# Optimization experiments

Hardware: AMD Instinct MI355X
Metric: run time of the kernel (lower is better)

The kernel has to match this reference:

```python
import jax, jax.numpy as jnp
import numpy as np

B_SZ, SEQ, D_MODEL = 2, 4096, 2048
EXPAND, D_STATE, D_CONV = 2, 16, 4
D_INNER = EXPAND * D_MODEL          # 4096
DT_RANK = -(-D_MODEL // 16)         # 128


def setup_inputs() -> dict:
    key = jax.random.key(0)
    ks = jax.random.split(key, 9)
    s = 0.02
    hidden_states = jax.random.normal(ks[0], (B_SZ, SEQ, D_MODEL), jnp.float32)
    W_in = jax.random.normal(ks[1], (2 * D_INNER, D_MODEL), jnp.float32) * s
    conv_w = jax.random.normal(ks[2], (D_INNER, D_CONV), jnp.float32) * 0.2
    conv_b = jnp.zeros((D_INNER,), jnp.float32)
    W_x = jax.random.normal(ks[3], (DT_RANK + 2 * D_STATE, D_INNER), jnp.float32) * s
    W_dt = jax.random.normal(ks[4], (D_INNER, DT_RANK), jnp.float32) * (DT_RANK ** -0.5)
    # dt bias so softplus(dt) ~ [1e-3, 0.1] as in Mamba init
    u = jax.random.uniform(ks[5], (D_INNER,), jnp.float32)
    dt = jnp.exp(u * (np.log(0.1) - np.log(1e-3)) + np.log(1e-3))
    dt_bias = dt + jnp.log(-jnp.expm1(-dt))  # inverse softplus
    # S4D-real init: A = -[1..d_state] per channel (kept negative for stability)
    A = -jnp.tile(jnp.arange(1.0, D_STATE + 1.0, dtype=jnp.float32), (D_INNER, 1))
    D = jnp.ones((D_INNER,), jnp.float32)
    W_out = jax.random.normal(ks[6], (D_MODEL, D_INNER), jnp.float32) * s
    return {"hidden_states": hidden_states, "W_in": W_in, "conv_w": conv_w,
            "conv_b": conv_b, "W_x": W_x, "W_dt": W_dt, "dt_bias": dt_bias,
            "A": A, "D": D, "W_out": W_out}


def _mamba_fwd(hidden_states, W_in, conv_w, conv_b, W_x, W_dt, dt_bias, A, D, W_out):
    # in_proj -> (B, L, 2*d_inner); split into x and gate z
    xz = jnp.einsum('bld,ed->ble', hidden_states, W_in)
    x, z = jnp.split(xz, 2, axis=-1)                    # (B,L,d_inner) each
    # causal depthwise conv1d over L (kernel d_conv), then SiLU
    d_conv = conv_w.shape[1]
    xp = jnp.pad(x, ((0, 0), (d_conv - 1, 0), (0, 0)))
    L = x.shape[1]
    xc = conv_b
    acc = jnp.zeros_like(x)
    for k in range(d_conv):                             # small fixed loop (4 taps)
        acc = acc + xp[:, k:k + L, :] * conv_w[:, k]
    x = jax.nn.silu(acc + conv_b)
    # x_proj -> dt_rank + 2*d_state
    ssm = jnp.einsum('bld,ed->ble', x, W_x)
    dt_r, Bm, Cm = jnp.split(ssm, [DT_RANK, DT_RANK + D_STATE], axis=-1)
    delta = jax.nn.softplus(jnp.einsum('blr,dr->bld', dt_r, W_dt) + dt_bias)
    # selective scan: h_t = exp(delta_t*A) h_{t-1} + delta_t*B_t*u_t ; y_t = C_t.h_t
    def step(state, inp):
        d_t, u_t, B_t, C_t = inp                        # (B,Di),(B,Di),(B,N),(B,N)
        dA = jnp.exp(d_t[..., None] * A)                # (B,Di,N)
        state = state * dA + (d_t * u_t)[..., None] * B_t[:, None, :]
        y = jnp.einsum('bdn,bn->bd', state, C_t)
        return state, y
    init = jnp.zeros((x.shape[0], D_INNER, D_STATE), jnp.float32)
    xs = (jnp.swapaxes(delta, 0, 1), jnp.swapaxes(x, 0, 1),
          jnp.swapaxes(Bm, 0, 1), jnp.swapaxes(Cm, 0, 1))
    _, ys = jax.lax.scan(step, init, xs)
    y = jnp.swapaxes(ys, 0, 1) + x * D                  # D skip connection
    y = y * jax.nn.silu(z)                              # gate
    return jnp.einsum('bld,md->blm', y, W_out)


def reference(hidden_states, W_in, conv_w, conv_b, W_x, W_dt, dt_bias, A, D, W_out):
    return _mamba_fwd(hidden_states, W_in, conv_w, conv_b, W_x, W_dt,
                      dt_bias, A, D, W_out)
```

## Files before the change

### kernel.cpp

```cpp
#include <hip/hip_runtime.h>
#include <hip/hip_bf16.h>
#include <cstdint>
#include <cstddef>

typedef _Float16 f16x8 __attribute__((ext_vector_type(8)));
typedef _Float16 f16x4 __attribute__((ext_vector_type(4)));
typedef float    f32x4 __attribute__((ext_vector_type(4)));

#define AS1 __attribute__((address_space(1)))
#define AS3 __attribute__((address_space(3)))

static constexpr int B_SZ = 2, SEQ = 4096, D_MODEL = 2048;
static constexpr int D_INNER = 4096, D_STATE = 16, D_CONV = 4, DT_RANK = 128;
static constexpr int M_ROWS = B_SZ * SEQ;
static constexpr int SSM_W  = DT_RANK + 2 * D_STATE;

__global__ __launch_bounds__(256) void k_cvt_f16(const float* __restrict__ in,
                                                 _Float16* __restrict__ out, int n4) {
    int i = blockIdx.x * 256 + threadIdx.x;
    if (i >= n4) return;
    f32x4 v = ((const f32x4*)in)[i];
    f16x4 h;
    h[0] = (_Float16)v[0]; h[1] = (_Float16)v[1];
    h[2] = (_Float16)v[2]; h[3] = (_Float16)v[3];
    ((f16x4*)out)[i] = h;
}

__global__ __launch_bounds__(256) void k_extract_dtr(const float* __restrict__ ssm,
                                                     _Float16* __restrict__ dtr) {
    int idx = blockIdx.x * 256 + threadIdx.x;
    if (idx >= M_ROWS * (DT_RANK / 4)) return;
    int m  = idx >> 5;
    int j4 = (idx & 31) * 4;
    f32x4 v = *(const f32x4*)&ssm[(size_t)m * SSM_W + j4];
    f16x4 h;
    h[0] = (_Float16)v[0]; h[1] = (_Float16)v[1];
    h[2] = (_Float16)v[2]; h[3] = (_Float16)v[3];
    *(f16x4*)&dtr[(size_t)m * DT_RANK + j4] = h;
}

template <int EPI>
__global__ __launch_bounds__(512, 2) void k_gemm256p(
    const _Float16* __restrict__ A, const _Float16* __restrict__ Bm, int K, int nby,
    void* __restrict__ out0, void* __restrict__ out1, int ldc) {
    __shared__ _Float16 lA[2][256][64];
    __shared__ _Float16 lB[2][256][64];
    constexpr int LBUF  = 32768;
    constexpr int LBUFH = 16384;

    const int tid = threadIdx.x, l = tid & 63, w = tid >> 6;
    const int fr = l & 15, fq = l >> 4;
    const int wrA = (w >> 2) * 128;
    const int wcB = (w & 3) * 64;

    const int nwg = gridDim.x, qq = nwg >> 3;
    const int id = (blockIdx.x & 7) * qq + (blockIdx.x >> 3);
    const int by = id % nby, bx = id / nby;
    const int tileM = by * 256, tileN = bx * 256;

    const int rsub = l >> 3;
    const int gco  = ((l & 7) ^ rsub) << 3;
    const int swz0 = (fq ^ (fr & 7)) << 4;

    const char* cA = (const char*)lA;
    const char* cB = (const char*)lB;
    const int bA0 = (wrA + fr) * 128 + swz0;
    const int bA1 = bA0 ^ 64;
    const int bB0 = (wcB + fr) * 128 + swz0;
    const int bB1 = bB0 ^ 64;

    const _Float16* pA[4];
    const _Float16* pB[4];
    _Float16* dA[4];
    _Float16* dB[4];
#pragma unroll
    for (int u = 0; u < 4; ++u) {
        const int brow = (u >> 1) * 128 + (w * 2 + (u & 1)) * 8;
        pA[u] = A  + (size_t)(tileM + brow + rsub) * K + gco;
        pB[u] = Bm + (size_t)(tileN + brow + rsub) * K + gco;
        dA[u] = &lA[0][brow][0];
        dB[u] = &lB[0][brow][0];
    }

    const int NK = K >> 6;

    f32x4 acc[8][4];
#pragma unroll
    for (int m = 0; m < 8; m++)
#pragma unroll
        for (int n = 0; n < 4; n++) acc[m][n] = (f32x4)0.f;

#pragma unroll
    for (int t = 0; t < 2; ++t) {
#pragma unroll
        for (int u = 0; u < 4; ++u)
            __builtin_amdgcn_global_load_lds((const AS1 void*)(pA[u] + t * 64),
                (AS3 void*)(dA[u] + t * LBUFH), 16, 0, 0);
#pragma unroll
        for (int u = 0; u < 4; ++u)
            __builtin_amdgcn_global_load_lds((const AS1 void*)(pB[u] + t * 64),
                (AS3 void*)(dB[u] + t * LBUFH), 16, 0, 0);
    }
#pragma unroll
    for (int u = 0; u < 4; ++u) { pA[u] += 128; pB[u] += 128; }
    asm volatile("s_waitcnt vmcnt(8)" ::: "memory");
    __builtin_amdgcn_s_barrier();

    f16x8 af[4][2], bf0[2][2], bf1[2][2];

#define MFMA_QUAD(MO, NO, BF)                                                        \
    __builtin_amdgcn_s_setprio(1);                                                   \
    _Pragma("unroll") for (int m = 0; m < 4; ++m)                                    \
    _Pragma("unroll") for (int n = 0; n < 2; ++n)                                    \
    _Pragma("unroll") for (int kk = 0; kk < 2; ++kk)                                 \
        acc[(MO) + m][(NO) + n] = __builtin_amdgcn_mfma_f32_16x16x32_f16(            \
            af[m][kk], BF[n][kk], acc[(MO) + m][(NO) + n], 0, 0, 0);                 \
    __builtin_amdgcn_s_setprio(0);

#define KTILE(BUF, KOFF, PF, DOEND)                                                  \
    _Pragma("unroll")                                                                \
    for (int m = 0; m < 4; ++m) {                                                    \
        af[m][0] = *(const f16x8*)(cA + (BUF) * LBUF + bA0 + m * 2048);              \
        af[m][1] = *(const f16x8*)(cA + (BUF) * LBUF + bA1 + m * 2048);              \
    }                                                                                \
    _Pragma("unroll")                                                                \
    for (int n = 0; n < 2; ++n) {                                                    \
        bf0[n][0] = *(const f16x8*)(cB + (BUF) * LBUF + bB0 + n * 2048);             \
        bf0[n][1] = *(const f16x8*)(cB + (BUF) * LBUF + bB1 + n * 2048);             \
    }                                                                                \
    __builtin_amdgcn_s_barrier();                                                    \
    asm volatile("s_waitcnt lgkmcnt(0)" ::: "memory");                               \
    __builtin_amdgcn_sched_barrier(0);                                               \
    MFMA_QUAD(0, 0, bf0)                                                             \
    __builtin_amdgcn_s_barrier();                                                    \
    _Pragma("unroll")                                                                \
    for (int n = 0; n < 2; ++n) {                                                    \
        bf1[n][0] = *(const f16x8*)(cB + (BUF) * LBUF + bB0 + (n + 2) * 2048);       \
        bf1[n][1] = *(const f16x8*)(cB + (BUF) * LBUF + bB1 + (n + 2) * 2048);       \
    }                                                                                \
    __builtin_amdgcn_s_barrier();                                                    \
    asm volatile("s_waitcnt lgkmcnt(0)" ::: "memory");                               \
    __builtin_amdgcn_sched_barrier(0);                                               \
    MFMA_QUAD(0, 2, bf1)                                                             \
    __builtin_amdgcn_s_barrier();                                                    \
    _Pragma("unroll")                                                                \
    for (int m = 0; m < 4; ++m) {                                                    \
        af[m][0] = *(const f16x8*)(cA + (BUF) * LBUF + bA0 + (m + 4) * 2048);        \
        af[m][1] = *(const f16x8*)(cA + (BUF) * LBUF + bA1 + (m + 4) * 2048);        \
    }                                                                                \
    if (PF) {                                                                        \
        _Pragma("unroll")                                                            \
        for (int u = 0; u < 4; ++u)                                                  \
            __builtin_amdgcn_global_load_lds((const AS1 void*)(pB[u] + (KOFF)),      \
                (AS3 void*)(dB[u] + (BUF) * LBUFH), 16, 0, 0);                       \
    }                                                                                \
    __builtin_amdgcn_s_barrier();                                                    \
    asm volatile("s_waitcnt lgkmcnt(0)" ::: "memory");                               \
    __builtin_amdgcn_sched_barrier(0);                                               \
    MFMA_QUAD(4, 0, bf0)                                                             \
    __builtin_amdgcn_s_barrier();                                                    \
    if (PF) {                                                                        \
        _Pragma("unroll")                                                            \
        for (int u = 0; u < 4; ++u)                                                  \
            __builtin_amdgcn_global_load_lds((const AS1 void*)(pA[u] + (KOFF)),      \
                (AS3 void*)(dA[u] + (BUF) * LBUFH), 16, 0, 0);                       \
    }                                                                                \
    __builtin_amdgcn_s_barrier();                                                    \
    MFMA_QUAD(4, 2, bf1)                                                             \
    if (DOEND) {                                                                     \
        if (PF) { asm volatile("s_waitcnt vmcnt(8)" ::: "memory"); }                 \
        else    { asm volatile("s_waitcnt vmcnt(0)" ::: "memory"); }                 \
        __builtin_amdgcn_s_barrier();                                                \
    }

    for (int kt = 0; kt < NK; kt += 2) {
        const bool pf0 = (kt + 2 < NK);
        const bool pf1 = (kt + 3 < NK);
        KTILE(0, 0, pf0, true)
        KTILE(1, 64, pf1, pf0)
#pragma unroll
        for (int u = 0; u < 4; ++u) { pA[u] += 128; pB[u] += 128; }
    }
#undef KTILE
#undef MFMA_QUAD

#pragma unroll
    for (int m = 0; m < 8; ++m) {
#pragma unroll
        for (int n = 0; n < 4; ++n) {
            const int r0 = tileM + wrA + m * 16 + fq * 4;
            const int c  = tileN + wcB + n * 16 + fr;
#pragma unroll
            for (int q = 0; q < 4; ++q) {
                const float  v  = acc[m][n][q];
                const size_t mm = (size_t)(r0 + q);
                if (EPI == 0) {
                    if (c < D_INNER)
                        ((_Float16*)out0)[mm * D_INNER + c] = (_Float16)v;
                    else
                        ((_Float16*)out1)[mm * D_INNER + (c - D_INNER)] = (_Float16)v;
                } else {
                    ((float*)out0)[mm * ldc + c] = v;
                }
            }
        }
    }
}

template <int BM, int BN, int EPI>
__global__ __launch_bounds__(256) void k_gemm_nt(
    const _Float16* __restrict__ A, const _Float16* __restrict__ Bm, int K,
    int lda, int ldb, void* __restrict__ out0,
    const float* __restrict__ bias, int ldc) {
    __shared__ _Float16 a_lds[BM][32];
    __shared__ _Float16 b_lds[BN][32];
    constexpr int MR = BM / 32;
    constexpr int NR = BN / 32;
    const int tid  = threadIdx.x;
    const int lane = tid & 63;
    const int wid  = tid >> 6;
    const int wr = wid >> 1, wc = wid & 1;
    const int tileM = blockIdx.y * BM;
    const int tileN = blockIdx.x * BN;

    f32x4 acc[MR][NR];
    for (int i = 0; i < MR; i++)
        for (int j = 0; j < NR; j++) acc[i][j] = (f32x4)0.f;

    constexpr int IS_A = BM / 16;
    constexpr int IS_B = BN / 16;
    const int srow = lane >> 2;
    const int skof = (lane & 3) * 8;
    const int fr = lane & 15, fq = lane >> 4;

    for (int kk = 0; kk < K; kk += 32) {
        if (kk) __syncthreads();
        for (int is = wid; is < IS_A + IS_B; is += 4) {
            const bool isA = is < IS_A;
            const int  li  = isA ? is : is - IS_A;
            const int  row = li * 16 + srow;
            const _Float16* g =
                isA ? (A  + (size_t)(tileM + row) * lda + kk + skof)
                    : (Bm + (size_t)(tileN + row) * ldb + kk + skof);
            char* lp = ((char*)(isA ? &a_lds[0][0] : &b_lds[0][0])) + (size_t)li * 1024;
            __builtin_amdgcn_global_load_lds((const AS1 void*)g, (AS3 void*)lp, 16, 0, 0);
        }
        __syncthreads();

        f16x8 af[MR], bf[NR];
#pragma unroll
        for (int i = 0; i < MR; i++)
            af[i] = *(const f16x8*)&a_lds[wr * (BM / 2) + i * 16 + fr][fq * 8];
#pragma unroll
        for (int j = 0; j < NR; j++)
            bf[j] = *(const f16x8*)&b_lds[wc * (BN / 2) + j * 16 + fr][fq * 8];
#pragma unroll
        for (int i = 0; i < MR; i++)
#pragma unroll
            for (int j = 0; j < NR; j++)
                acc[i][j] = __builtin_amdgcn_mfma_f32_16x16x32_f16(af[i], bf[j], acc[i][j], 0, 0, 0);
    }

#pragma unroll
    for (int i = 0; i < MR; i++) {
#pragma unroll
        for (int j = 0; j < NR; j++) {
            const int r0 = tileM + wr * (BM / 2) + i * 16 + fq * 4;
            const int c  = tileN + wc * (BN / 2) + j * 16 + fr;
#pragma unroll
            for (int q = 0; q < 4; q++) {
                const float  v = acc[i][j][q];
                const size_t m = (size_t)(r0 + q);
                if (EPI == 1) {
                    ((float*)out0)[m * ldc + c] = v;
                } else {
                    float x  = v + bias[c];
                    float sp = (x > 20.f) ? x : log1pf(__expf(x));
                    ((_Float16*)out0)[m * ldc + c] = (_Float16)sp;
                }
            }
        }
    }
}

__global__ __launch_bounds__(256) void k_conv_silu(const _Float16* __restrict__ x,
                                                   const float* __restrict__ w,
                                                   const float* __restrict__ bias,
                                                   _Float16* __restrict__ out) {
    const int idx = blockIdx.x * 256 + threadIdx.x;
    const int d4 = idx & (D_INNER / 4 - 1);
    const int t  = (idx >> 10) & (SEQ - 1);
    const int b  = idx >> 22;
    const int d  = d4 * 4;
    const size_t rowbase = (size_t)b * SEQ * D_INNER;

    f32x4 wv[4];
#pragma unroll
    for (int i = 0; i < 4; i++) wv[i] = ((const f32x4*)w)[d + i];

    float acc[4];
#pragma unroll
    for (int i = 0; i < 4; i++) acc[i] = bias[d + i];
#pragma unroll
    for (int k = 0; k < D_CONV; k++) {
        int ti = t - (D_CONV - 1) + k;
        if (ti < 0) continue;
        f16x4 xv = *(const f16x4*)&x[rowbase + (size_t)ti * D_INNER + d];
#pragma unroll
        for (int i = 0; i < 4; i++) acc[i] += (float)xv[i] * wv[i][k];
    }
    f16x4 o;
#pragma unroll
    for (int i = 0; i < 4; i++) {
        float v = acc[i];
        o[i] = (_Float16)(v / (1.f + __expf(-v)));
    }
    *(f16x4*)&out[rowbase + (size_t)t * D_INNER + d] = o;
}

template <int CH, typename ST>
__global__ __launch_bounds__(256) void k_scan_p1(const _Float16* __restrict__ delta_h,
                                                 const _Float16* __restrict__ xc,
                                                 const float* __restrict__ ssm,
                                                 const float* __restrict__ Aptr,
                                                 ST* __restrict__ Sbuf,
                                                 ST* __restrict__ Pbuf) {
    constexpr int NCH = SEQ / CH;
    constexpr float L2E = 1.44269504088896f;
    const int bid   = blockIdx.x;
    const int dg    = bid & 15;
    const int chunk = (bid >> 4) % NCH;
    const int b     = bid / (16 * NCH);
    const int d     = dg * 256 + threadIdx.x;

    __shared__ float bsh[CH][D_STATE];
    const size_t rb = (size_t)b * SEQ + (size_t)chunk * CH;
    for (int i = threadIdx.x; i < CH * D_STATE; i += 256) {
        int t = i >> 4, n = i & 15;
        bsh[t][n] = ssm[(rb + t) * SSM_W + DT_RANK + n];
    }
    __syncthreads();

    float a2[D_STATE];
#pragma unroll
    for (int n = 0; n < D_STATE; n++) a2[n] = Aptr[(size_t)d * D_STATE + n] * L2E;
    float st[D_STATE];
#pragma unroll
    for (int n = 0; n < D_STATE; n++) st[n] = 0.f;
    float dtsum = 0.f;

    for (int t = 0; t < CH; ++t) {
        const size_t idx = (rb + t) * D_INNER + d;
        const float dt = (float)delta_h[idx];
        const float u  = (float)xc[idx];
        const float du = dt * u;
        dtsum += dt;
#pragma unroll
        for (int n = 0; n < D_STATE; n++) {
            float p = exp2f(dt * a2[n]);
            st[n] = st[n] * p + du * bsh[t][n];
        }
    }
    const size_t ob = ((size_t)(b * NCH + chunk) * D_STATE) * D_INNER + d;
#pragma unroll
    for (int n = 0; n < D_STATE; n++) {
        Sbuf[ob + (size_t)n * D_INNER] = (ST)st[n];
        Pbuf[ob + (size_t)n * D_INNER] = (ST)exp2f(dtsum * a2[n]);
    }
}

template <int NCH, typename ST>
__global__ __launch_bounds__(256) void k_scan_p2(ST* __restrict__ Sbuf,
                                                 const ST* __restrict__ Pbuf) {
    const int id = blockIdx.x * 256 + threadIdx.x;
    const int d = id & (D_INNER - 1);
    const int n = (id >> 12) & 15;
    const int b = id >> 16;
    float h = 0.f;
    for (int c = 0; c < NCH; ++c) {
        const size_t off = ((size_t)((b * NCH + c) * D_STATE + n)) * D_INNER + d;
        const float Pv = (float)Pbuf[off];
        const float Sv = (float)Sbuf[off];
        Sbuf[off] = (ST)h;
        h = Pv * h + Sv;
    }
}

template <int CH, typename ST>
__global__ __launch_bounds__(256) void k_scan_p3(const _Float16* __restrict__ delta_h,
                                                 const _Float16* __restrict__ xc,
                                                 const float* __restrict__ ssm,
                                                 const _Float16* __restrict__ z,
                                                 const float* __restrict__ Aptr,
                                                 const float* __restrict__ Dptr,
                                                 const ST* __restrict__ Sbuf,
                                                 _Float16* __restrict__ y_out) {
    constexpr int NCH = SEQ / CH;
    constexpr float L2E = 1.44269504088896f;
    const int bid   = blockIdx.x;
    const int dg    = bid & 15;
    const int chunk = (bid >> 4) % NCH;
    const int b     = bid / (16 * NCH);
    const int d     = dg * 256 + threadIdx.x;

    __shared__ float bsh[CH][2 * D_STATE];
    const size_t rb = (size_t)b * SEQ + (size_t)chunk * CH;
    for (int i = threadIdx.x; i < CH * 2 * D_STATE; i += 256) {
        int t = i >> 5, j = i & 31;
        bsh[t][j] = ssm[(rb + t) * SSM_W + DT_RANK + j];
    }
    __syncthreads();

    float a2[D_STATE];
#pragma unroll
    for (int n = 0; n < D_STATE; n++) a2[n] = Aptr[(size_t)d * D_STATE + n] * L2E;
    const float Dd = Dptr[d];

    const size_t ob = ((size_t)(b * NCH + chunk) * D_STATE) * D_INNER + d;
    float st[D_STATE];
#pragma unroll
    for (int n = 0; n < D_STATE; n++) st[n] = (float)Sbuf[ob + (size_t)n * D_INNER];

    for (int t = 0; t < CH; ++t) {
        const size_t idx = (rb + t) * D_INNER + d;
        const float dt = (float)delta_h[idx];
        const float u  = (float)xc[idx];
        const float du = dt * u;
        float y = 0.f;
#pragma unroll
        for (int n = 0; n < D_STATE; n++) {
            float p = exp2f(dt * a2[n]);
            st[n] = st[n] * p + du * bsh[t][n];
            y += st[n] * bsh[t][D_STATE + n];
        }
        const float zv = (float)z[idx];
        const float g  = zv / (1.f + __expf(-zv));
        y_out[idx] = (_Float16)((y + u * Dd) * g);
    }
}

__global__ __launch_bounds__(256) void k_scan(const _Float16* __restrict__ delta_h,
                                              const _Float16* __restrict__ xc,
                                              const float* __restrict__ ssm,
                                              const _Float16* __restrict__ z,
                                              const float* __restrict__ Aptr,
                                              const float* __restrict__ Dptr,
                                              _Float16* __restrict__ y_out) {
    const int b = blockIdx.x >> 4;
    const int d = (blockIdx.x & 15) * 256 + threadIdx.x;
    constexpr float L2E = 1.44269504088896f;
    float a2[D_STATE];
#pragma unroll
    for (int n = 0; n < D_STATE; n++) a2[n] = Aptr[(size_t)d * D_STATE + n] * L2E;
    const float Dd = Dptr[d];
    float st[D_STATE];
#pragma unroll
    for (int n = 0; n < D_STATE; n++) st[n] = 0.f;
    __shared__ float bc[128][32];
    const size_t rb = (size_t)b * SEQ;
    for (int tc = 0; tc < SEQ; tc += 128) {
        __syncthreads();
        for (int i = threadIdx.x; i < 128 * 32; i += 256) {
            int tl = i >> 5, j = i & 31;
            bc[tl][j] = ssm[(rb + tc + tl) * SSM_W + DT_RANK + j];
        }
        __syncthreads();
        for (int tl = 0; tl < 128; ++tl) {
            const size_t idx = (rb + tc + tl) * D_INNER + d;
            const float dt = (float)delta_h[idx];
            const float u  = (float)xc[idx];
            const float du = dt * u;
            float y = 0.f;
#pragma unroll
            for (int n = 0; n < D_STATE; n++) {
                float dA = exp2f(dt * a2[n]);
                st[n] = st[n] * dA + du * bc[tl][n];
                y += st[n] * bc[tl][D_STATE + n];
            }
            const float zv = (float)z[idx];
            const float g  = zv / (1.f + __expf(-zv));
            y_out[idx] = (_Float16)((y + u * Dd) * g);
        }
    }
}

template <int CH, typename ST>
static void launch_chunked_scan(const _Float16* delta_h, const _Float16* xc,
                                const float* ssm, const _Float16* z,
                                const float* Aptr, const float* Dptr,
                                ST* S, ST* P, _Float16* y, hipStream_t stream) {
    constexpr int NCH = SEQ / CH;
    k_scan_p1<CH, ST><<<B_SZ * NCH * 16, 256, 0, stream>>>(delta_h, xc, ssm, Aptr, S, P);
    k_scan_p2<NCH, ST><<<(B_SZ * 16 * D_INNER) / 256, 256, 0, stream>>>(S, P);
    k_scan_p3<CH, ST><<<B_SZ * NCH * 16, 256, 0, stream>>>(delta_h, xc, ssm, z, Aptr, Dptr, S, y);
}

extern "C" void kernel_launch(void* const* d_in, const int* in_sizes, int n_in,
                              void* d_out, int out_size, void* d_ws, size_t ws_size,
                              hipStream_t stream) {
    const float* hs    = (const float*)d_in[0];
    const float* W_in  = (const float*)d_in[1];
    const float* convw = (const float*)d_in[2];
    const float* convb = (const float*)d_in[3];
    const float* W_x   = (const float*)d_in[4];
    const float* W_dt  = (const float*)d_in[5];
    const float* dtb   = (const float*)d_in[6];
    const float* Aptr  = (const float*)d_in[7];
    const float* Dptr  = (const float*)d_in[8];
    const float* W_out = (const float*)d_in[9];

    char* ws = (char*)d_ws;
    _Float16* hs_h    = (_Float16*)(ws + 0);
    _Float16* Win_h   = (_Float16*)(ws + 33554432);
    _Float16* y_h     = (_Float16*)(ws + 0);
    _Float16* xraw    = (_Float16*)(ws + 67108864);
    _Float16* delta_h = (_Float16*)(ws + 67108864);
    _Float16* xc      = (_Float16*)(ws + 134217728);
    float*    ssm     = (float*)   (ws + 201326592);
    _Float16* dtr     = (_Float16*)(ws + 206569472);
    _Float16* Wx_h    = (_Float16*)(ws + 208666624);
    _Float16* Wdt_h   = (_Float16*)(ws + 209977344);
    _Float16* Wout_h  = (_Float16*)(ws + 211025920);
    _Float16* z_h     = (_Float16*)d_out;
    const size_t spbase = 227803136ull;

    auto cvt = [&](const float* in, _Float16* out, int n) {
        int n4 = n / 4;
        k_cvt_f16<<<(n4 + 255) / 256, 256, 0, stream>>>(in, out, n4);
    };
    cvt(hs,    hs_h,   B_SZ * SEQ * D_MODEL);
    cvt(W_in,  Win_h,  2 * D_INNER * D_MODEL);
    cvt(W_x,   Wx_h,   SSM_W * D_INNER);
    cvt(W_dt,  Wdt_h,  D_INNER * DT_RANK);
    cvt(W_out, Wout_h, D_MODEL * D_INNER);

    k_gemm256p<0><<<(M_ROWS / 256) * (2 * D_INNER / 256), 512, 0, stream>>>(
        hs_h, Win_h, D_MODEL, M_ROWS / 256, xraw, z_h, 0);

    k_conv_silu<<<(B_SZ * SEQ * (D_INNER / 4)) / 256, 256, 0, stream>>>(xraw, convw, convb, xc);

    k_gemm_nt<128, 32, 1><<<dim3(SSM_W / 32, M_ROWS / 128), 256, 0, stream>>>(
        xc, Wx_h, D_INNER, D_INNER, D_INNER, ssm, nullptr, SSM_W);

    k_extract_dtr<<<(M_ROWS * (DT_RANK / 4)) / 256, 256, 0, stream>>>(ssm, dtr);

    k_gemm_nt<128, 128, 2><<<dim3(D_INNER / 128, M_ROWS / 128), 256, 0, stream>>>(
        dtr, Wdt_h, DT_RANK, DT_RANK, DT_RANK, delta_h, dtb, D_INNER);

    {
        const size_t e64  = (size_t)B_SZ * (SEQ / 64)  * D_STATE * D_INNER;
        const size_t e128 = (size_t)B_SZ * (SEQ / 128) * D_STATE * D_INNER;
        if (ws_size >= spbase + 2 * e64 * sizeof(float)) {
            float* S = (float*)(ws + spbase);
            float* P = S + e64;
            launch_chunked_scan<64, float>(delta_h, xc, ssm, z_h, Aptr, Dptr, S, P, y_h, stream);
        } else if (ws_size >= spbase + 2 * e128 * sizeof(float)) {
            float* S = (float*)(ws + spbase);
            float* P = S + e128;
            launch_chunked_scan<128, float>(delta_h, xc, ssm, z_h, Aptr, Dptr, S, P, y_h, stream);
        } else if (ws_size >= spbase + 2 * e128 * sizeof(_Float16)) {
            _Float16* S = (_Float16*)(ws + spbase);
            _Float16* P = S + e128;
            launch_chunked_scan<128, _Float16>(delta_h, xc, ssm, z_h, Aptr, Dptr, S, P, y_h, stream);
        } else {
            k_scan<<<B_SZ * (D_INNER / 256), 256, 0, stream>>>(delta_h, xc, ssm, z_h, Aptr, Dptr, y_h);
        }
    }

    k_gemm256p<1><<<(M_ROWS / 256) * (D_MODEL / 256), 512, 0, stream>>>(
        y_h, Wout_h, D_INNER, M_ROWS / 256, d_out, nullptr, D_MODEL);
}
```

Before: 1.131 ms.

## Load GEMM B operand directly from global into registers, drop LDS B tiles

Changes the 256x256 fp16 GEMM so each wave loads its B fragments straight from global memory into registers (double-buffered in registers), leaving only A staged through LDS. The A pipeline becomes a single-buffered prefetch into the alternate buffer with fewer barriers and split-K fragment loads. This halves LDS use and removes many barriers. In exchange, B reads from global are uncoalesced and duplicated across the waves sharing columns, and register pressure rises. The vmcnt counting has also changed, so the synchronization is fragile.

Measured after the change: 2.186 ms. 1.93x slower.

```diff
diff --git a/kernel.cpp b/kernel.cpp
--- a/kernel.cpp
+++ b/kernel.cpp
@@ -44,7 +44,6 @@
     const _Float16* __restrict__ A, const _Float16* __restrict__ Bm, int K, int nby,
     void* __restrict__ out0, void* __restrict__ out1, int ldc) {
     __shared__ _Float16 lA[2][256][64];
-    __shared__ _Float16 lB[2][256][64];
     constexpr int LBUF  = 32768;
     constexpr int LBUFH = 16384;
 
@@ -61,26 +60,22 @@
     const int rsub = l >> 3;
     const int gco  = ((l & 7) ^ rsub) << 3;
     const int swz0 = (fq ^ (fr & 7)) << 4;
-
     const char* cA = (const char*)lA;
-    const char* cB = (const char*)lB;
     const int bA0 = (wrA + fr) * 128 + swz0;
     const int bA1 = bA0 ^ 64;
-    const int bB0 = (wcB + fr) * 128 + swz0;
-    const int bB1 = bB0 ^ 64;
 
     const _Float16* pA[4];
-    const _Float16* pB[4];
     _Float16* dA[4];
-    _Float16* dB[4];
 #pragma unroll
     for (int u = 0; u < 4; ++u) {
         const int brow = (u >> 1) * 128 + (w * 2 + (u & 1)) * 8;
-        pA[u] = A  + (size_t)(tileM + brow + rsub) * K + gco;
-        pB[u] = Bm + (size_t)(tileN + brow + rsub) * K + gco;
+        pA[u] = A + (size_t)(tileM + brow + rsub) * K + gco;
         dA[u] = &lA[0][brow][0];
-        dB[u] = &lB[0][brow][0];
-    }
+    }
+    const AS1 _Float16* pBf[4];
+#pragma unroll
+    for (int n = 0; n < 4; ++n)
+        pBf[n] = (const AS1 _Float16*)(Bm + (size_t)(tileN + wcB + n * 16 + fr) * K + fq * 8);
 
     const int NK = K >> 6;
 
@@ -90,99 +85,77 @@
 #pragma unroll
         for (int n = 0; n < 4; n++) acc[m][n] = (f32x4)0.f;
 
-#pragma unroll
-    for (int t = 0; t < 2; ++t) {
-#pragma unroll
-        for (int u = 0; u < 4; ++u)
-            __builtin_amdgcn_global_load_lds((const AS1 void*)(pA[u] + t * 64),
-                (AS3 void*)(dA[u] + t * LBUFH), 16, 0, 0);
-#pragma unroll
-        for (int u = 0; u < 4; ++u)
-            __builtin_amdgcn_global_load_lds((const AS1 void*)(pB[u] + t * 64),
-                (AS3 void*)(dB[u] + t * LBUFH), 16, 0, 0);
-    }
-#pragma unroll
-    for (int u = 0; u < 4; ++u) { pA[u] += 128; pB[u] += 128; }
+    f16x8 af0[8], af1[8], bfA[4][2], bfB[4][2];
+
+#pragma unroll
+    for (int u = 0; u < 4; ++u)
+        __builtin_amdgcn_global_load_lds((const AS1 void*)pA[u], (AS3 void*)dA[u], 16, 0, 0);
+#pragma unroll
+    for (int n = 0; n < 4; ++n) {
+        bfA[n][0] = *(const AS1 f16x8*)(pBf[n]);
+        bfA[n][1] = *(const AS1 f16x8*)(pBf[n] + 32);
+    }
+#pragma unroll
+    for (int u = 0; u < 4; ++u) pA[u] += 64;
+#pragma unroll
+    for (int n = 0; n < 4; ++n) pBf[n] += 64;
     asm volatile("s_waitcnt vmcnt(8)" ::: "memory");
     __builtin_amdgcn_s_barrier();
 
-    f16x8 af[4][2], bf0[2][2], bf1[2][2];
-
-#define MFMA_QUAD(MO, NO, BF)                                                        \
+#define MFMA16(AF, MO, BF, KK)                                                       \
     __builtin_amdgcn_s_setprio(1);                                                   \
     _Pragma("unroll") for (int m = 0; m < 4; ++m)                                    \
-    _Pragma("unroll") for (int n = 0; n < 2; ++n)                                    \
-    _Pragma("unroll") for (int kk = 0; kk < 2; ++kk)                                 \
-        acc[(MO) + m][(NO) + n] = __builtin_amdgcn_mfma_f32_16x16x32_f16(            \
-            af[m][kk], BF[n][kk], acc[(MO) + m][(NO) + n], 0, 0, 0);                 \
+    _Pragma("unroll") for (int n = 0; n < 4; ++n)                                    \
+        acc[(MO) + m][n] = __builtin_amdgcn_mfma_f32_16x16x32_f16(                   \
+            AF[(MO) + m], BF[n][KK], acc[(MO) + m][n], 0, 0, 0);                     \
     __builtin_amdgcn_s_setprio(0);
 
-#define KTILE(BUF, KOFF, PF, DOEND)                                                  \
+#define KTILE(BUF, BFC, BFN, PF, KOFF)                                               \
     _Pragma("unroll")                                                                \
-    for (int m = 0; m < 4; ++m) {                                                    \
-        af[m][0] = *(const f16x8*)(cA + (BUF) * LBUF + bA0 + m * 2048);              \
-        af[m][1] = *(const f16x8*)(cA + (BUF) * LBUF + bA1 + m * 2048);              \
-    }                                                                                \
-    _Pragma("unroll")                                                                \
-    for (int n = 0; n < 2; ++n) {                                                    \
-        bf0[n][0] = *(const f16x8*)(cB + (BUF) * LBUF + bB0 + n * 2048);             \
-        bf0[n][1] = *(const f16x8*)(cB + (BUF) * LBUF + bB1 + n * 2048);             \
-    }                                                                                \
-    __builtin_amdgcn_s_barrier();                                                    \
-    asm volatile("s_waitcnt lgkmcnt(0)" ::: "memory");                               \
-    __builtin_amdgcn_sched_barrier(0);                                               \
-    MFMA_QUAD(0, 0, bf0)                                                             \
-    __builtin_amdgcn_s_barrier();                                                    \
-    _Pragma("unroll")                                                                \
-    for (int n = 0; n < 2; ++n) {                                                    \
-        bf1[n][0] = *(const f16x8*)(cB + (BUF) * LBUF + bB0 + (n + 2) * 2048);       \
-        bf1[n][1] = *(const f16x8*)(cB + (BUF) * LBUF + bB1 + (n + 2) * 2048);       \
-    }                                                                                \
-    __builtin_amdgcn_s_barrier();                                                    \
-    asm volatile("s_waitcnt lgkmcnt(0)" ::: "memory");                               \
-    __builtin_amdgcn_sched_barrier(0);                                               \
-    MFMA_QUAD(0, 2, bf1)                                                             \
-    __builtin_amdgcn_s_barrier();                                                    \
-    _Pragma("unroll")                                                                \
-    for (int m = 0; m < 4; ++m) {                                                    \
-        af[m][0] = *(const f16x8*)(cA + (BUF) * LBUF + bA0 + (m + 4) * 2048);        \
-        af[m][1] = *(const f16x8*)(cA + (BUF) * LBUF + bA1 + (m + 4) * 2048);        \
-    }                                                                                \
-    if (PF) {                                                                        \
-        _Pragma("unroll")                                                            \
-        for (int u = 0; u < 4; ++u)                                                  \
-            __builtin_amdgcn_global_load_lds((const AS1 void*)(pB[u] + (KOFF)),      \
-                (AS3 void*)(dB[u] + (BUF) * LBUFH), 16, 0, 0);                       \
-    }                                                                                \
-    __builtin_amdgcn_s_barrier();                                                    \
-    asm volatile("s_waitcnt lgkmcnt(0)" ::: "memory");                               \
-    __builtin_amdgcn_sched_barrier(0);                                               \
-    MFMA_QUAD(4, 0, bf0)                                                             \
-    __builtin_amdgcn_s_barrier();                                                    \
+    for (int m = 0; m < 8; ++m)                                                      \
+        af0[m] = *(const f16x8*)(cA + (BUF) * LBUF + bA0 + m * 2048);                \
     if (PF) {                                                                        \
         _Pragma("unroll")                                                            \
         for (int u = 0; u < 4; ++u)                                                  \
             __builtin_amdgcn_global_load_lds((const AS1 void*)(pA[u] + (KOFF)),      \
-                (AS3 void*)(dA[u] + (BUF) * LBUFH), 16, 0, 0);                       \
+                (AS3 void*)(dA[u] + (1 - (BUF)) * LBUFH), 16, 0, 0);                 \
     }                                                                                \
-    __builtin_amdgcn_s_barrier();                                                    \
-    MFMA_QUAD(4, 2, bf1)                                                             \
-    if (DOEND) {                                                                     \
-        if (PF) { asm volatile("s_waitcnt vmcnt(8)" ::: "memory"); }                 \
-        else    { asm volatile("s_waitcnt vmcnt(0)" ::: "memory"); }                 \
+    asm volatile("s_waitcnt lgkmcnt(4)" ::: "memory");                               \
+    __builtin_amdgcn_sched_barrier(0);                                               \
+    MFMA16(af0, 0, BFC, 0)                                                           \
+    _Pragma("unroll")                                                                \
+    for (int m = 0; m < 8; ++m)                                                      \
+        af1[m] = *(const f16x8*)(cA + (BUF) * LBUF + bA1 + m * 2048);                \
+    asm volatile("s_waitcnt lgkmcnt(8)" ::: "memory");                               \
+    __builtin_amdgcn_sched_barrier(0);                                               \
+    MFMA16(af0, 4, BFC, 0)                                                           \
+    if (PF) {                                                                        \
+        _Pragma("unroll")                                                            \
+        for (int n = 0; n < 4; ++n) {                                                \
+            BFN[n][0] = *(const AS1 f16x8*)(pBf[n] + (KOFF));                        \
+            BFN[n][1] = *(const AS1 f16x8*)(pBf[n] + (KOFF) + 32);                   \
+        }                                                                            \
+    }                                                                                \
+    asm volatile("s_waitcnt lgkmcnt(0)" ::: "memory");                               \
+    __builtin_amdgcn_sched_barrier(0);                                               \
+    MFMA16(af1, 0, BFC, 1)                                                           \
+    MFMA16(af1, 4, BFC, 1)                                                           \
+    if (PF) {                                                                        \
+        asm volatile("s_waitcnt vmcnt(8)" ::: "memory");                             \
         __builtin_amdgcn_s_barrier();                                                \
     }
 
     for (int kt = 0; kt < NK; kt += 2) {
-        const bool pf0 = (kt + 2 < NK);
-        const bool pf1 = (kt + 3 < NK);
-        KTILE(0, 0, pf0, true)
-        KTILE(1, 64, pf1, pf0)
-#pragma unroll
-        for (int u = 0; u < 4; ++u) { pA[u] += 128; pB[u] += 128; }
+        const bool pf1 = (kt + 2 < NK);
+        KTILE(0, bfA, bfB, true, 0)
+        KTILE(1, bfB, bfA, pf1, 64)
+#pragma unroll
+        for (int u = 0; u < 4; ++u) pA[u] += 128;
+#pragma unroll
+        for (int n = 0; n < 4; ++n) pBf[n] += 128;
     }
 #undef KTILE
-#undef MFMA_QUAD
+#undef MFMA16
 
 #pragma unroll
     for (int m = 0; m < 8; ++m) {
```

## Restructure GEMM k-tile into k-half phases with partial LDS waits and fewer barriers

Applied to the files above, without the earlier changes.

Reorganizes the GEMM inner k-tile so each phase loads one k-half of the A and B fragments (8 A plus 4 B) and runs 16 MFMAs per group, rather than splitting by N quadrant. Partial lgkmcnt waits replace full waits, so later LDS reads overlap with earlier MFMAs. Most of the per-quad workgroup barriers are dropped. This lowers sync overhead and exposed LDS latency, but more fragments stay live, which raises register pressure, and the barrier placement around the prefetch into the same buffer is easy to get subtly wrong.

Result: slower. 1.916 ms (+69.5%).

```diff
diff --git a/kernel.cpp b/kernel.cpp
--- a/kernel.cpp
+++ b/kernel.cpp
@@ -61,7 +61,6 @@
     const int rsub = l >> 3;
     const int gco  = ((l & 7) ^ rsub) << 3;
     const int swz0 = (fq ^ (fr & 7)) << 4;
-
     const char* cA = (const char*)lA;
     const char* cB = (const char*)lB;
     const int bA0 = (wrA + fr) * 128 + swz0;
@@ -106,67 +105,65 @@
     asm volatile("s_waitcnt vmcnt(8)" ::: "memory");
     __builtin_amdgcn_s_barrier();
 
-    f16x8 af[4][2], bf0[2][2], bf1[2][2];
-
-#define MFMA_QUAD(MO, NO, BF)                                                        \
+    f16x8 af0[8], af1[8], bf0[4], bf1[4];
+
+#define MFMA16(AF, MO, BF)                                                           \
     __builtin_amdgcn_s_setprio(1);                                                   \
     _Pragma("unroll") for (int m = 0; m < 4; ++m)                                    \
-    _Pragma("unroll") for (int n = 0; n < 2; ++n)                                    \
-    _Pragma("unroll") for (int kk = 0; kk < 2; ++kk)                                 \
-        acc[(MO) + m][(NO) + n] = __builtin_amdgcn_mfma_f32_16x16x32_f16(            \
-            af[m][kk], BF[n][kk], acc[(MO) + m][(NO) + n], 0, 0, 0);                 \
+    _Pragma("unroll") for (int n = 0; n < 4; ++n)                                    \
+        acc[(MO) + m][n] = __builtin_amdgcn_mfma_f32_16x16x32_f16(                   \
+            AF[(MO) + m], BF[n], acc[(MO) + m][n], 0, 0, 0);                         \
     __builtin_amdgcn_s_setprio(0);
 
-#define KTILE(BUF, KOFF, PF, DOEND)                                                  \
+#define KTILE(BUF, PF, KOFF, DOEND)                                                  \
+                                               \
     _Pragma("unroll")                                                                \
-    for (int m = 0; m < 4; ++m) {                                                    \
-        af[m][0] = *(const f16x8*)(cA + (BUF) * LBUF + bA0 + m * 2048);              \
-        af[m][1] = *(const f16x8*)(cA + (BUF) * LBUF + bA1 + m * 2048);              \
-    }                                                                                \
+    for (int m = 0; m < 4; ++m)                                                      \
+        af0[m] = *(const f16x8*)(cA + (BUF) * LBUF + bA0 + m * 2048);                \
     _Pragma("unroll")                                                                \
-    for (int n = 0; n < 2; ++n) {                                                    \
-        bf0[n][0] = *(const f16x8*)(cB + (BUF) * LBUF + bB0 + n * 2048);             \
-        bf0[n][1] = *(const f16x8*)(cB + (BUF) * LBUF + bB1 + n * 2048);             \
-    }                                                                                \
-    __builtin_amdgcn_s_barrier();                                                    \
-    asm volatile("s_waitcnt lgkmcnt(0)" ::: "memory");                               \
+    for (int n = 0; n < 4; ++n)                                                      \
+        bf0[n] = *(const f16x8*)(cB + (BUF) * LBUF + bB0 + n * 2048);                \
+                                                       \
+    _Pragma("unroll")                                                                \
+    for (int m = 0; m < 4; ++m)                                                      \
+        af0[m + 4] = *(const f16x8*)(cA + (BUF) * LBUF + bA0 + (m + 4) * 2048);      \
+    asm volatile("s_waitcnt lgkmcnt(4)" ::: "memory");                               \
     __builtin_amdgcn_sched_barrier(0);                                               \
-    MFMA_QUAD(0, 0, bf0)                                                             \
-    __builtin_amdgcn_s_barrier();                                                    \
+    MFMA16(af0, 0, bf0)                                                              \
+                                               \
     _Pragma("unroll")                                                                \
-    for (int n = 0; n < 2; ++n) {                                                    \
-        bf1[n][0] = *(const f16x8*)(cB + (BUF) * LBUF + bB0 + (n + 2) * 2048);       \
-        bf1[n][1] = *(const f16x8*)(cB + (BUF) * LBUF + bB1 + (n + 2) * 2048);       \
-    }                                                                                \
-    __builtin_amdgcn_s_barrier();                                                    \
-    asm volatile("s_waitcnt lgkmcnt(0)" ::: "memory");                               \
+    for (int m = 0; m < 4; ++m)                                                      \
+        af1[m] = *(const f16x8*)(cA + (BUF) * LBUF + bA1 + m * 2048);                \
+    _Pragma("unroll")                                                                \
+    for (int n = 0; n < 4; ++n)                                                      \
+        bf1[n] = *(const f16x8*)(cB + (BUF) * LBUF + bB1 + n * 2048);                \
+    asm volatile("s_waitcnt lgkmcnt(8)" ::: "memory");                               \
     __builtin_amdgcn_sched_barrier(0);                                               \
-    MFMA_QUAD(0, 2, bf1)                                                             \
-    __builtin_amdgcn_s_barrier();                                                    \
+    MFMA16(af0, 4, bf0)                                                              \
+                                                       \
     _Pragma("unroll")                                                                \
-    for (int m = 0; m < 4; ++m) {                                                    \
-        af[m][0] = *(const f16x8*)(cA + (BUF) * LBUF + bA0 + (m + 4) * 2048);        \
-        af[m][1] = *(const f16x8*)(cA + (BUF) * LBUF + bA1 + (m + 4) * 2048);        \
-    }                                                                                \
+    for (int m = 0; m < 4; ++m)                                                      \
+        af1[m + 4] = *(const f16x8*)(cA + (BUF) * LBUF + bA1 + (m + 4) * 2048);      \
+    asm volatile("s_waitcnt lgkmcnt(4)" ::: "memory");                               \
+    __builtin_amdgcn_sched_barrier(0);                                               \
+    __builtin_amdgcn_s_barrier();                    \
     if (PF) {                                                                        \
         _Pragma("unroll")                                                            \
         for (int u = 0; u < 4; ++u)                                                  \
             __builtin_amdgcn_global_load_lds((const AS1 void*)(pB[u] + (KOFF)),      \
                 (AS3 void*)(dB[u] + (BUF) * LBUFH), 16, 0, 0);                       \
     }                                                                                \
-    __builtin_amdgcn_s_barrier();                                                    \
+    MFMA16(af1, 0, bf1)                                                              \
     asm volatile("s_waitcnt lgkmcnt(0)" ::: "memory");                               \
     __builtin_amdgcn_sched_barrier(0);                                               \
-    MFMA_QUAD(4, 0, bf0)                                                             \
-    __builtin_amdgcn_s_barrier();                                                    \
+    __builtin_amdgcn_s_barrier();                    \
     if (PF) {                                                                        \
         _Pragma("unroll")                                                            \
         for (int u = 0; u < 4; ++u)                                                  \
             __builtin_amdgcn_global_load_lds((const AS1 void*)(pA[u] + (KOFF)),      \
                 (AS3 void*)(dA[u] + (BUF) * LBUFH), 16, 0, 0);                       \
     }                                                                                \
-    __builtin_amdgcn_s_barrier();                                                    \
-    MFMA_QUAD(4, 2, bf1)                                                             \
+    MFMA16(af1, 4, bf1)                                                              \
     if (DOEND) {                                                                     \
         if (PF) { asm volatile("s_waitcnt vmcnt(8)" ::: "memory"); }                 \
         else    { asm volatile("s_waitcnt vmcnt(0)" ::: "memory"); }                 \
@@ -176,13 +173,13 @@
     for (int kt = 0; kt < NK; kt += 2) {
         const bool pf0 = (kt + 2 < NK);
         const bool pf1 = (kt + 3 < NK);
-        KTILE(0, 0, pf0, true)
-        KTILE(1, 64, pf1, pf0)
+        KTILE(0, pf0, 0, true)
+        KTILE(1, pf1, 64, pf0)
 #pragma unroll
         for (int u = 0; u < 4; ++u) { pA[u] += 128; pB[u] += 128; }
     }
 #undef KTILE
-#undef MFMA_QUAD
+#undef MFMA16
 
 #pragma unroll
     for (int m = 0; m < 8; ++m) {
```
